# Kernel optimization log

Measured on AMD Instinct MI355X. Metric: run time of the kernel, lower is better.

## Reference

```python
import jax, jax.numpy as jnp
import numpy as np

B, C, E, K, HW = 8, 64, 4, 2, 128
LEAK = 0.2      # LeakyReLU slope in gate and experts
CLAMP = 0.8     # InvBlock clamp
EPS = 1e-5      # InstanceNorm eps


def _conv(x, w, b, pad):
    # x: [B,Ci,H,W], w: [Co,Ci,kh,kw] (OIHW)
    y = jax.lax.conv_general_dilated(x, w, (1, 1), [(pad, pad), (pad, pad)],
                                     dimension_numbers=('NCHW', 'OIHW', 'NCHW'))
    return y + b[None, :, None, None]


def _inorm(x, g, b):
    # InstanceNorm2d: per-sample, per-channel over H,W; biased variance
    m = x.mean(axis=(2, 3), keepdims=True)
    v = x.var(axis=(2, 3), keepdims=True)
    return (x - m) / jnp.sqrt(v + EPS) * g[None, :, None, None] + b[None, :, None, None]


def _hin(x, w1, b1, nw, nb, w2, b2):
    # HinResBlock with relu_slope=1 (d=1 passed by InvBlock) -> activations are identity
    r = _conv(x, w1, b1, 1)
    h1, h2 = jnp.split(r, 2, axis=1)
    r = jnp.concatenate([_inorm(h1, nw, nb), h2], axis=1)
    r = _conv(r, w2, b2, 1)
    return x + r


def setup_inputs() -> dict:
    key = jax.random.key(0)
    ks = jax.random.split(key, 20)
    s = 0.05
    Ch = C // 2
    inp = {
        'x': jax.random.normal(ks[0], (B, 2 * C, HW, HW), jnp.float32),
        # invertible 1x1 conv weight [2C, 2C]
        'winv': jax.random.normal(ks[1], (2 * C, 2 * C), jnp.float32) * s,
        # stacked HinResBlock params for F (idx 0), G (idx 1), H (idx 2)
        'blk_w1': jax.random.normal(ks[2], (3, C, C, 3, 3), jnp.float32) * s,
        'blk_b1': jax.random.normal(ks[3], (3, C), jnp.float32) * s,
        'blk_nw': jnp.ones((3, Ch), jnp.float32),
        'blk_nb': jnp.zeros((3, Ch), jnp.float32),
        'blk_w2': jax.random.normal(ks[4], (3, C, C, 3, 3), jnp.float32) * s,
        'blk_b2': jax.random.normal(ks[5], (3, C), jnp.float32) * s,
        # fuse 1x1 conv 2C -> C
        'fuse_w': jax.random.normal(ks[6], (C, 2 * C, 1, 1), jnp.float32) * s,
        'fuse_b': jax.random.normal(ks[7], (C,), jnp.float32) * s,
        # gate: fc0 (noise) random; fc1 weight zero-init per source, bias random
        'gw0': jax.random.normal(ks[8], (E, C), jnp.float32) * s,
        'gb0': jax.random.normal(ks[9], (E,), jnp.float32) * s,
        'gw1': jnp.zeros((E, C), jnp.float32),
        'gb1': jax.random.normal(ks[10], (E,), jnp.float32) * s,
        # stacked expert ConvProce params
        'ew1': jax.random.normal(ks[11], (E, C, C, 3, 3), jnp.float32) * s,
        'eb1': jax.random.normal(ks[12], (E, C), jnp.float32) * s,
        'ew2': jax.random.normal(ks[13], (E, C, C, 3, 3), jnp.float32) * s,
        'eb2': jax.random.normal(ks[14], (E, C), jnp.float32) * s,
    }
    return inp


def _forward(x, winv, blk_w1, blk_b1, blk_nw, blk_nb, blk_w2, blk_b2,
             fuse_w, fuse_b, gw0, gb0, gw1, gb1, ew1, eb1, ew2, eb2):
    # --- pre_fuse: InvBlock(2C, C) then 1x1 conv 2C->C ---
    z = jnp.einsum('oi,bihw->bohw', winv, x)  # invertible 1x1 conv (logdet unused)
    x1, x2 = z[:, :C], z[:, C:]
    hin = lambda i, h: _hin(h, blk_w1[i], blk_b1[i], blk_nw[i], blk_nb[i], blk_w2[i], blk_b2[i])
    y1 = x1 + hin(0, x2)                         # F
    s = CLAMP * (jax.nn.sigmoid(hin(2, y1)) * 2.0 - 1.0)  # H
    y2 = x2 * jnp.exp(s) + hin(1, y1)            # G
    xf = _conv(jnp.concatenate([y1, y2], axis=1), fuse_w, fuse_b, 0)  # [B,C,H,W]

    # --- gate ---
    g = jnp.max(xf, axis=(2, 3)) + jnp.mean(xf, axis=(2, 3))  # [B,C]
    lg = jax.nn.leaky_relu(g @ gw1.T + gb1, LEAK)             # [B,E]
    noise = jax.nn.softplus(g @ gw0.T + gb0)
    nm = noise.mean(axis=1, keepdims=True)
    ns = jnp.std(noise, axis=1, ddof=1, keepdims=True)        # torch.std is unbiased
    norm_noise = (noise - nm) / ns
    _, idx = jax.lax.top_k(lg + norm_noise, K)                # [B,K]
    mask = jnp.zeros((B, E), lg.dtype).at[jnp.arange(B)[:, None], idx].set(1.0)
    cof = jax.nn.softmax(jnp.where(mask > 0, lg, -jnp.inf), axis=1)  # [B,E]

    # --- experts: dense weighted combine (non-topk gates are exactly 0) ---
    def expert(w1, b1, w2, b2):
        h = jax.nn.leaky_relu(_conv(xf, w1, b1, 1), LEAK)
        return _conv(h, w2, b2, 1) + xf
    eouts = jax.vmap(expert)(ew1, eb1, ew2, eb2)  # [E,B,C,H,W]
    out = jnp.einsum('ebchw,be->bchw', eouts, cof)
    return out, cof


def reference(x, winv, blk_w1, blk_b1, blk_nw, blk_nb, blk_w2, blk_b2,
              fuse_w, fuse_b, gw0, gb0, gw1, gb1, ew1, eb1, ew2, eb2):
    return _forward(x, winv, blk_w1, blk_b1, blk_nw, blk_nb, blk_w2, blk_b2,
                    fuse_w, fuse_b, gw0, gb0, gw1, gb1, ew1, eb1, ew2, eb2)
```

## Files before the change

kernel.cpp:

```cpp
#include <hip/hip_runtime.h>
#include <cstddef>


#define HW2 16384
typedef short short8 __attribute__((ext_vector_type(8)));
typedef float f32x4 __attribute__((ext_vector_type(4)));
typedef unsigned short ushort_t;
typedef unsigned int uint_t;

enum { M_PLAIN = 0, M_ADD2 = 1, M_SIGEXP = 2, M_COUPLE = 3, M_LRELU = 4, M_EACC = 5 };

__device__ __forceinline__ float bf2f(ushort_t u) {
  return __uint_as_float(((uint_t)u) << 16);
}
__device__ __forceinline__ ushort_t f2bf(float f) {
  uint_t u = __float_as_uint(f);
  u += 0x7fffu + ((u >> 16) & 1u);
  return (ushort_t)(u >> 16);
}
__device__ __forceinline__ uint_t pack2(float a, float b) {
  return (uint_t)f2bf(a) | ((uint_t)f2bf(b) << 16);
}
__device__ __forceinline__ void ld4bf(const ushort_t* p, float* o) {
  uint2 d = *(const uint2*)p;
  o[0] = bf2f((ushort_t)(d.x & 0xffff)); o[1] = bf2f((ushort_t)(d.x >> 16));
  o[2] = bf2f((ushort_t)(d.y & 0xffff)); o[3] = bf2f((ushort_t)(d.y >> 16));
}
__device__ __forceinline__ void st4bf(ushort_t* p, const float* v) {
  uint2 st; st.x = pack2(v[0], v[1]); st.y = pack2(v[2], v[3]);
  *(uint2*)p = st;
}
__device__ __forceinline__ void gload_lds16(const void* g, void* l) {
  __builtin_amdgcn_global_load_lds(
      (const __attribute__((address_space(1))) void*)g,
      (__attribute__((address_space(3))) void*)l, 16, 0, 0);
}

__global__ void wtrans_kernel(const float* __restrict__ bw1, const float* __restrict__ bw2,
                              const float* __restrict__ ew1, const float* __restrict__ ew2,
                              ushort_t* __restrict__ wbuf) {
  int idx = blockIdx.x * 256 + threadIdx.x;
  int ci = idx & 63; int co = (idx >> 6) & 63;
  int rest = idx >> 12;
  int tap = rest % 9; int conv = rest / 9;
  const float* src;
  if (conv < 3)       src = bw1 + (size_t)conv * 36864;
  else if (conv < 6)  src = bw2 + (size_t)(conv - 3) * 36864;
  else if (conv < 10) src = ew1 + (size_t)(conv - 6) * 36864;
  else                src = ew2 + (size_t)(conv - 10) * 36864;
  float v = src[(co * 64 + ci) * 9 + tap];
  int n = co >> 4, col = co & 15;
  int h = ci >> 5, krow = (ci >> 3) & 3, e = ci & 7;
  int pos = conv * 36864 + (((tap * 2 + h) * 4 + n) << 9) + ((col << 2) + krow) * 8 + e;
  wbuf[pos] = f2bf(v);
}

__global__ void cvt_kernel(const float* __restrict__ s, ushort_t* __restrict__ d, int n) {
  int i = blockIdx.x * 256 + threadIdx.x;
  if (i < n) d[i] = f2bf(s[i]);
}

__global__ __launch_bounds__(256) void xtrans_kernel(const float* __restrict__ x,
                                                     ushort_t* __restrict__ xh) {
  int b = blockIdx.y;
  int oct = blockIdx.x >> 6;
  int p = ((blockIdx.x & 63) << 8) + threadIdx.x;
  short8 v;
#pragma unroll
  for (int j = 0; j < 8; ++j)
    v[j] = (short)f2bf(x[((size_t)(b * 128 + oct * 8 + j)) * HW2 + p]);
  *(short8*)(xh + ((size_t)b * HW2 + p) * 128 + oct * 8) = v;
}

template <int MODE, bool INORM>
__global__ __launch_bounds__(256, 3) void conv3_kernel(
    const ushort_t* __restrict__ in, int icstr, int icoff,
    const ushort_t* __restrict__ wgt, const float* __restrict__ bias,
    void* __restrict__ outv, int ocstr, int ocoff,
    const ushort_t* __restrict__ r1, int r1cstr, int r1off,
    const ushort_t* __restrict__ r2, int r2cstr, int r2off,
    const ushort_t* __restrict__ mul, int mcstr, int moff,
    const float* __restrict__ kh, const float* __restrict__ cof, int expert) {
  int b = blockIdx.y;
  float cv = 0.f; bool first = false;
  if (MODE == M_LRELU || MODE == M_EACC) {
    cv = cof[b * 4 + expert];
    if (cv == 0.f) return;
    if (MODE == M_EACC) {
      first = true;
      for (int e2 = 0; e2 < expert; ++e2) if (cof[b * 4 + e2] != 0.f) first = false;
    }
  }
  int tile = blockIdx.x;
  int ty0 = (tile >> 3) << 4;
  int tx0 = (tile & 7) << 4;
  int t = threadIdx.x;
  int lane = t & 63, w = t >> 6;

  __shared__ __align__(16) ushort_t sm[2592 * 8];
  char* smb = (char*)sm;

  if (!INORM) {
    for (int j = t; j < 2592; j += 256) {
      int row = j / 144, rem = j - row * 144;
      int xx = rem >> 3;
      int gy = ty0 + row - 1, gx = tx0 + xx - 1;
      if ((unsigned)gy >= 128u || (unsigned)gx >= 128u) {
        short8 z = {0, 0, 0, 0, 0, 0, 0, 0};
        *(short8*)(smb + (j << 4)) = z;
      }
    }
    for (int k = w; k < 41; k += 4) {
      int j = (k << 6) + lane;
      int row = j / 144, rem = j - row * 144;
      int xx = rem >> 3, octS = rem & 7;
      int oct = octS ^ (xx & 7);
      int gy = ty0 + row - 1, gx = tx0 + xx - 1;
      if (j < 2592 && (unsigned)gy < 128u && (unsigned)gx < 128u) {
        const ushort_t* gp =
            in + ((size_t)b * HW2 + (gy << 7) + gx) * icstr + icoff + oct * 8;
        gload_lds16(gp, smb + (k << 10));
      }
    }
  } else {
    short8 v[11];
#pragma unroll
    for (int k = 0; k < 11; ++k) {
      int j = t + (k << 8);
      short8 vv = {0, 0, 0, 0, 0, 0, 0, 0};
      if (j < 2592) {
        int row = j / 144, rem = j - row * 144;
        int xx = rem >> 3, octS = rem & 7;
        int oct = octS ^ (xx & 7);
        int gy = ty0 + row - 1, gx = tx0 + xx - 1;
        if ((unsigned)gy < 128u && (unsigned)gx < 128u) {
          vv = *(const short8*)(in + ((size_t)b * HW2 + (gy << 7) + gx) * icstr + icoff + oct * 8);
          if (oct < 4) {
            const float* khp = kh + (b * 32 + oct * 8) * 2;
#pragma unroll
            for (int jq = 0; jq < 8; ++jq) {
              float f = bf2f((ushort_t)vv[jq]);
              vv[jq] = (short)f2bf(f * khp[jq * 2] + khp[jq * 2 + 1]);
            }
          }
        }
      }
      v[k] = vv;
    }
#pragma unroll
    for (int k = 0; k < 11; ++k) {
      int j = t + (k << 8);
      if (j < 2592) *(short8*)(smb + (j << 4)) = v[k];
    }
  }
  __syncthreads();

  int col = lane & 15, krow = lane >> 4;
  int wofs = ((col << 2) + krow) * 8;
  f32x4 acc[4][4] = {};

#pragma unroll
  for (int tap = 0; tap < 9; ++tap) {
    const int dy = tap / 3, dx = tap - dy * 3;
#pragma unroll
    for (int h = 0; h < 2; ++h) {
      short8 af[4];
      const ushort_t* wbase = wgt + (((tap * 2 + h) * 4) << 9) + wofs;
#pragma unroll
      for (int n = 0; n < 4; ++n) af[n] = *(const short8*)(wbase + (n << 9));
      short8 bfr[4];
#pragma unroll
      for (int s = 0; s < 4; ++s) {
        int row = (w << 2) + s + dy, xx = col + dx;
        bfr[s] = *(const short8*)(smb +
                 (((row * 18 + xx) * 8 + ((h * 4 + krow) ^ (xx & 7))) << 4));
      }
#pragma unroll
      for (int s = 0; s < 4; ++s)
#pragma unroll
        for (int n = 0; n < 4; ++n)
          acc[s][n] = __builtin_amdgcn_mfma_f32_16x16x32_bf16(af[n], bfr[s], acc[s][n], 0, 0, 0);
    }
  }

#pragma unroll
  for (int s = 0; s < 4; ++s) {
    int py = ty0 + (w << 2) + s;
    size_t pix = (size_t)b * HW2 + (py << 7) + tx0 + col;
#pragma unroll
    for (int n = 0; n < 4; ++n) {
      int cb = n * 16 + krow * 4;
      float v[4];
#pragma unroll
      for (int r = 0; r < 4; ++r) v[r] = acc[s][n][r] + bias[cb + r];
      if (MODE == M_PLAIN) {
        st4bf((ushort_t*)outv + pix * ocstr + ocoff + cb, v);
      } else if (MODE == M_ADD2) {
        float a[4], bb[4];
        ld4bf(r1 + pix * r1cstr + r1off + cb, a);
        ld4bf(r2 + pix * r2cstr + r2off + cb, bb);
#pragma unroll
        for (int r = 0; r < 4; ++r) v[r] += a[r] + bb[r];
        st4bf((ushort_t*)outv + pix * ocstr + ocoff + cb, v);
      } else if (MODE == M_SIGEXP) {
        float a[4];
        ld4bf(r1 + pix * r1cstr + r1off + cb, a);
#pragma unroll
        for (int r = 0; r < 4; ++r) {
          float tt = v[r] + a[r];
          float sg = 1.f / (1.f + __expf(-tt));
          v[r] = __expf(1.6f * sg - 0.8f);
        }
        st4bf((ushort_t*)outv + pix * ocstr + ocoff + cb, v);
      } else if (MODE == M_COUPLE) {
        float a[4], bb[4], mm[4];
        ld4bf(r1 + pix * r1cstr + r1off + cb, a);
        ld4bf(r2 + pix * r2cstr + r2off + cb, bb);
        ld4bf(mul + pix * mcstr + moff + cb, mm);
#pragma unroll
        for (int r = 0; r < 4; ++r) v[r] += a[r] + bb[r] * mm[r];
        st4bf((ushort_t*)outv + pix * ocstr + ocoff + cb, v);
      } else if (MODE == M_LRELU) {
#pragma unroll
        for (int r = 0; r < 4; ++r) v[r] = v[r] > 0.f ? v[r] : 0.2f * v[r];
        st4bf((ushort_t*)outv + pix * ocstr + ocoff + cb, v);
      } else if (MODE == M_EACC) {
        float a[4];
        ld4bf(r1 + pix * r1cstr + r1off + cb, a);
        f32x4 val;
#pragma unroll
        for (int r = 0; r < 4; ++r) val[r] = cv * (v[r] + a[r]);
        float* ap = (float*)outv + pix * 64 + cb;
        if (first) *(f32x4*)ap = val;
        else { f32x4 old = *(f32x4*)ap; *(f32x4*)ap = old + val; }
      }
    }
  }
}

template <int NF>
__global__ __launch_bounds__(256, 3) void mm1_kernel(
    const ushort_t* __restrict__ in, int icstr,
    const ushort_t* __restrict__ wgt, const float* __restrict__ bias,
    ushort_t* __restrict__ out, int ocstr) {
  int b = blockIdx.y;
  int p0 = blockIdx.x << 7;
  int t = threadIdx.x, lane = t & 63, w = t >> 6;
  int col = lane & 15, krow = lane >> 4;
  size_t pixb = (size_t)b * HW2 + p0 + w * 32;
  short8 bfr[4][2];
#pragma unroll
  for (int kk = 0; kk < 4; ++kk)
#pragma unroll
    for (int s = 0; s < 2; ++s)
      bfr[kk][s] = *(const short8*)(in + (pixb + s * 16 + col) * icstr + kk * 32 + krow * 8);
  f32x4 acc[2][NF] = {};
#pragma unroll
  for (int kk = 0; kk < 4; ++kk) {
#pragma unroll
    for (int n = 0; n < NF; ++n) {
      short8 af = *(const short8*)(wgt + (n * 16 + col) * 128 + kk * 32 + krow * 8);
#pragma unroll
      for (int s = 0; s < 2; ++s)
        acc[s][n] = __builtin_amdgcn_mfma_f32_16x16x32_bf16(af, bfr[kk][s], acc[s][n], 0, 0, 0);
    }
  }
#pragma unroll
  for (int s = 0; s < 2; ++s) {
    size_t pix = pixb + s * 16 + col;
#pragma unroll
    for (int n = 0; n < NF; ++n) {
      int cb = n * 16 + krow * 4;
      float v[4];
#pragma unroll
      for (int r = 0; r < 4; ++r) v[r] = acc[s][n][r] + (bias ? bias[cb + r] : 0.f);
      st4bf(out + pix * ocstr + cb, v);
    }
  }
}

__global__ __launch_bounds__(256) void ireduce_kernel(const ushort_t* __restrict__ h,
                                                      float* __restrict__ part) {
  int b = blockIdx.y, chunk = blockIdx.x, t = threadIdx.x;
  int c = t & 31, g = t >> 5;
  float s = 0.f, q = 0.f;
  const ushort_t* base = h + ((size_t)b * HW2 + chunk * 512) * 64 + c;
  for (int i = 0; i < 64; ++i) {
    float f = bf2f(base[(g + i * 8) * 64]);
    s += f; q += f * f;
  }
  __shared__ float ls[8][32], lq[8][32];
  ls[g][c] = s; lq[g][c] = q;
  __syncthreads();
  if (t < 32) {
    float S = 0.f, Q = 0.f;
    for (int gg = 0; gg < 8; ++gg) { S += ls[gg][t]; Q += lq[gg][t]; }
    float* pp = part + ((b * 32 + chunk) * 32 + t) * 2;
    pp[0] = S; pp[1] = Q;
  }
}

__global__ void istat_kernel(const float* __restrict__ part, const float* __restrict__ nw,
                             const float* __restrict__ nb, float* __restrict__ kh) {
  int t = threadIdx.x; if (t >= 256) return;
  int b = t >> 5, c = t & 31;
  float S = 0.f, Q = 0.f;
  for (int ch = 0; ch < 32; ++ch) {
    const float* pp = part + ((b * 32 + ch) * 32 + c) * 2;
    S += pp[0]; Q += pp[1];
  }
  float m = S * (1.f / 16384.f);
  float var = Q * (1.f / 16384.f) - m * m;
  float k = nw[c] * rsqrtf(var + 1e-5f);
  kh[(b * 32 + c) * 2] = k;
  kh[(b * 32 + c) * 2 + 1] = nb[c] - m * k;
}

__global__ __launch_bounds__(256) void preduce_kernel(const ushort_t* __restrict__ xf,
                                                      float* __restrict__ part2) {
  int b = blockIdx.y, chunk = blockIdx.x, t = threadIdx.x;
  int c = t & 63, g = t >> 6;
  float s = 0.f, mx = -3.4e38f;
  const ushort_t* base = xf + ((size_t)b * HW2 + chunk * 512) * 64 + c;
  for (int i = 0; i < 128; ++i) {
    float f = bf2f(base[(g + i * 4) * 64]);
    s += f; mx = fmaxf(mx, f);
  }
  __shared__ float ls[4][64], lm[4][64];
  ls[g][c] = s; lm[g][c] = mx;
  __syncthreads();
  if (t < 64) {
    float S = ls[0][t] + ls[1][t] + ls[2][t] + ls[3][t];
    float M = fmaxf(fmaxf(lm[0][t], lm[1][t]), fmaxf(lm[2][t], lm[3][t]));
    float* pp = part2 + ((b * 32 + chunk) * 64 + t) * 2;
    pp[0] = S; pp[1] = M;
  }
}

__global__ void pool2_kernel(const float* __restrict__ part2, float* __restrict__ g) {
  int t = blockIdx.x * blockDim.x + threadIdx.x;
  if (t >= 512) return;
  int b = t >> 6, c = t & 63;
  float S = 0.f, M = -3.4e38f;
  for (int ch = 0; ch < 32; ++ch) {
    const float* pp = part2 + ((b * 32 + ch) * 64 + c) * 2;
    S += pp[0]; M = fmaxf(M, pp[1]);
  }
  g[t] = M + S * (1.f / 16384.f);
}

__global__ void gate_kernel(const float* __restrict__ g, const float* __restrict__ gw0,
                            const float* __restrict__ gb0, const float* __restrict__ gw1,
                            const float* __restrict__ gb1, float* __restrict__ cof) {
  int b = threadIdx.x;
  if (b >= 8) return;
  float lg[4], noise[4];
  for (int e = 0; e < 4; ++e) {
    float a0 = gb0[e], a1 = gb1[e];
    for (int c = 0; c < 64; ++c) {
      float gv = g[b * 64 + c];
      a0 += gv * gw0[e * 64 + c];
      a1 += gv * gw1[e * 64 + c];
    }
    lg[e] = a1 > 0.f ? a1 : 0.2f * a1;
    noise[e] = fmaxf(a0, 0.f) + log1pf(expf(-fabsf(a0)));
  }
  float nm = 0.25f * (noise[0] + noise[1] + noise[2] + noise[3]);
  float vs = 0.f;
  for (int e = 0; e < 4; ++e) { float d = noise[e] - nm; vs += d * d; }
  float ns = sqrtf(vs / 3.f);
  float sc[4];
  for (int e = 0; e < 4; ++e) sc[e] = lg[e] + (noise[e] - nm) / ns;
  int i1 = 0;
  for (int e = 1; e < 4; ++e) if (sc[e] > sc[i1]) i1 = e;
  int i2 = -1;
  for (int e = 0; e < 4; ++e) if (e != i1 && (i2 < 0 || sc[e] > sc[i2])) i2 = e;
  float mx = fmaxf(lg[i1], lg[i2]);
  float e1 = expf(lg[i1] - mx), e2 = expf(lg[i2] - mx);
  float d = e1 + e2;
  for (int e = 0; e < 4; ++e) cof[b * 4 + e] = 0.f;
  cof[b * 4 + i1] = e1 / d;
  cof[b * 4 + i2] = e2 / d;
}

__global__ __launch_bounds__(256) void nchw_kernel(const float* __restrict__ acc,
                                                   float* __restrict__ out) {
  int b = blockIdx.y, pix0 = blockIdx.x << 6, t = threadIdx.x;
  __shared__ float ts[64][68];
  for (int i = t; i < 1024; i += 256) {
    int px = i >> 4, grp = i & 15;
    f32x4 v = *(const f32x4*)(acc + ((size_t)b * HW2 + pix0 + px) * 64 + grp * 4);
    *(f32x4*)(&ts[px][grp * 4]) = v;
  }
  __syncthreads();
  int c = t >> 2, xg = t & 3;
#pragma unroll
  for (int j = 0; j < 4; ++j) {
    int px = xg * 16 + j * 4;
    f32x4 o;
#pragma unroll
    for (int k = 0; k < 4; ++k) o[k] = ts[px + k][c];
    *(f32x4*)(out + (((size_t)b * 64 + c) << 14) + pix0 + px) = o;
  }
}

extern "C" void kernel_launch(void* const* d_in, const int* in_sizes, int n_in,
                              void* d_out, int out_size, void* d_ws, size_t ws_size,
                              hipStream_t stream) {
  const float* x    = (const float*)d_in[0];
  const float* winv = (const float*)d_in[1];
  const float* w1   = (const float*)d_in[2];
  const float* b1   = (const float*)d_in[3];
  const float* nw   = (const float*)d_in[4];
  const float* nb   = (const float*)d_in[5];
  const float* w2   = (const float*)d_in[6];
  const float* b2   = (const float*)d_in[7];
  const float* fw   = (const float*)d_in[8];
  const float* fb   = (const float*)d_in[9];
  const float* gw0  = (const float*)d_in[10];
  const float* gb0  = (const float*)d_in[11];
  const float* gw1  = (const float*)d_in[12];
  const float* gb1  = (const float*)d_in[13];
  const float* ew1  = (const float*)d_in[14];
  const float* eb1  = (const float*)d_in[15];
  const float* ew2  = (const float*)d_in[16];
  const float* eb2  = (const float*)d_in[17];

  char* W = (char*)d_ws;
  ushort_t* A    = (ushort_t*)(W);
  ushort_t* Bz   = (ushort_t*)(W + 33554432);
  float*    accb = (float*)(W + 33554432);
  ushort_t* Ch   = (ushort_t*)(W + 67108864);
  ushort_t* Dx   = (ushort_t*)(W + 83886080);
  ushort_t* w3   = (ushort_t*)(W + 100663296);
  ushort_t* wmm  = (ushort_t*)(W + 101695488);
  ushort_t* wfu  = (ushort_t*)(W + 101728256);
  float* part1 = (float*)(W + 101744640);
  float* kh    = (float*)(W + 101810176);
  float* part2 = (float*)(W + 101812224);
  float* gbuf  = (float*)(W + 101943296);

  float* out = (float*)d_out;
  float* cof = out + (size_t)8 * 64 * HW2;

  const int WS3 = 36864;
  dim3 cg1(128, 8), cg3(64, 8), rg(32, 8);

  wtrans_kernel<<<2016, 256, 0, stream>>>(w1, w2, ew1, ew2, w3);
  cvt_kernel<<<64, 256, 0, stream>>>(winv, wmm, 16384);
  cvt_kernel<<<32, 256, 0, stream>>>(fw, wfu, 8192);
  xtrans_kernel<<<dim3(1024, 8), 256, 0, stream>>>(x, A);

  mm1_kernel<8><<<cg1, 256, 0, stream>>>(A, 128, wmm, nullptr, Bz, 128);

  conv3_kernel<M_PLAIN, false><<<cg3, 256, 0, stream>>>(Bz, 128, 64, w3 + 0 * WS3, b1,
      Ch, 64, 0, nullptr,0,0, nullptr,0,0, nullptr,0,0, kh, nullptr, 0);
  ireduce_kernel<<<rg, 256, 0, stream>>>(Ch, part1);
  istat_kernel<<<1, 256, 0, stream>>>(part1, nw, nb, kh);
  conv3_kernel<M_ADD2, true><<<cg3, 256, 0, stream>>>(Ch, 64, 0, w3 + 3 * WS3, b2,
      A, 128, 0, Bz, 128, 64, Bz, 128, 0, nullptr,0,0, kh, nullptr, 0);

  conv3_kernel<M_PLAIN, false><<<cg3, 256, 0, stream>>>(A, 128, 0, w3 + 2 * WS3, b1 + 128,
      Ch, 64, 0, nullptr,0,0, nullptr,0,0, nullptr,0,0, kh, nullptr, 0);
  ireduce_kernel<<<rg, 256, 0, stream>>>(Ch, part1);
  istat_kernel<<<1, 256, 0, stream>>>(part1, nw + 64, nb + 64, kh);
  conv3_kernel<M_SIGEXP, true><<<cg3, 256, 0, stream>>>(Ch, 64, 0, w3 + 5 * WS3, b2 + 128,
      Dx, 64, 0, A, 128, 0, nullptr,0,0, nullptr,0,0, kh, nullptr, 0);

  conv3_kernel<M_PLAIN, false><<<cg3, 256, 0, stream>>>(A, 128, 0, w3 + 1 * WS3, b1 + 64,
      Ch, 64, 0, nullptr,0,0, nullptr,0,0, nullptr,0,0, kh, nullptr, 0);
  ireduce_kernel<<<rg, 256, 0, stream>>>(Ch, part1);
  istat_kernel<<<1, 256, 0, stream>>>(part1, nw + 32, nb + 32, kh);
  conv3_kernel<M_COUPLE, true><<<cg3, 256, 0, stream>>>(Ch, 64, 0, w3 + 4 * WS3, b2 + 64,
      A, 128, 64, A, 128, 0, Bz, 128, 64, Dx, 64, 0, kh, nullptr, 0);

  mm1_kernel<4><<<cg1, 256, 0, stream>>>(A, 128, wfu, fb, Dx, 64);

  preduce_kernel<<<rg, 256, 0, stream>>>(Dx, part2);
  pool2_kernel<<<2, 256, 0, stream>>>(part2, gbuf);
  gate_kernel<<<1, 64, 0, stream>>>(gbuf, gw0, gb0, gw1, gb1, cof);

  for (int e = 0; e < 4; ++e) {
    conv3_kernel<M_LRELU, false><<<cg3, 256, 0, stream>>>(Dx, 64, 0, w3 + (6 + e) * WS3,
        eb1 + e * 64, Ch, 64, 0, nullptr,0,0, nullptr,0,0, nullptr,0,0, kh, cof, e);
    conv3_kernel<M_EACC, false><<<cg3, 256, 0, stream>>>(Ch, 64, 0, w3 + (10 + e) * WS3,
        eb2 + e * 64, (void*)accb, 64, 0, Dx, 64, 0, nullptr,0,0, nullptr,0,0, kh, cof, e);
  }

  nchw_kernel<<<dim3(256, 8), 256, 0, stream>>>(accb, out);
}
```

Measured before the change: 548.5 us.

## Give each wave a private halo tile in conv3 and drop block barrier

The 3x3 conv kernel now has each of its four waves stage its own 6x18-pixel halo region into a private slice of shared memory, instead of the whole block cooperatively loading one 18x18 tile. This removes the __syncthreads barrier, leaving only a per-wave vmcnt wait. In exchange the overlapping halo rows are loaded redundantly, shared memory per block grows from about 41KB to 55KB, and launch bounds drop from 3 to 2 blocks per CU for conv3 and mm1. The cost is lower occupancy and more global/LDS traffic.

```diff
diff --git a/kernel.cpp b/kernel.cpp
--- a/kernel.cpp
+++ b/kernel.cpp
@@ -73,7 +73,7 @@
 }
 
 template <int MODE, bool INORM>
-__global__ __launch_bounds__(256, 3) void conv3_kernel(
+__global__ __launch_bounds__(256, 2) void conv3_kernel(
     const ushort_t* __restrict__ in, int icstr, int icoff,
     const ushort_t* __restrict__ wgt, const float* __restrict__ bias,
     void* __restrict__ outv, int ocstr, int ocoff,
@@ -97,42 +97,51 @@
   int t = threadIdx.x;
   int lane = t & 63, w = t >> 6;
 
-  __shared__ __align__(16) ushort_t sm[2592 * 8];
-  char* smb = (char*)sm;
+  __shared__ __align__(16) ushort_t sm[4 * 864 * 8];
+  char* smb = (char*)sm + w * 13824;
+  int ry0 = ty0 + (w << 2) - 1;
 
   if (!INORM) {
-    for (int j = t; j < 2592; j += 256) {
-      int row = j / 144, rem = j - row * 144;
-      int xx = rem >> 3;
-      int gy = ty0 + row - 1, gx = tx0 + xx - 1;
-      if ((unsigned)gy >= 128u || (unsigned)gx >= 128u) {
-        short8 z = {0, 0, 0, 0, 0, 0, 0, 0};
-        *(short8*)(smb + (j << 4)) = z;
+#pragma unroll
+    for (int k = 0; k < 14; ++k) {
+      int j = (k << 6) + lane;
+      if (j < 864) {
+        int r = j / 144, rem = j - r * 144;
+        int xx = rem >> 3;
+        int gy = ry0 + r, gx = tx0 + xx - 1;
+        if ((unsigned)gy >= 128u || (unsigned)gx >= 128u) {
+          short8 z = {0, 0, 0, 0, 0, 0, 0, 0};
+          *(short8*)(smb + (j << 4)) = z;
+        }
       }
     }
-    for (int k = w; k < 41; k += 4) {
+#pragma unroll
+    for (int k = 0; k < 14; ++k) {
       int j = (k << 6) + lane;
-      int row = j / 144, rem = j - row * 144;
-      int xx = rem >> 3, octS = rem & 7;
-      int oct = octS ^ (xx & 7);
-      int gy = ty0 + row - 1, gx = tx0 + xx - 1;
-      if (j < 2592 && (unsigned)gy < 128u && (unsigned)gx < 128u) {
-        const ushort_t* gp =
-            in + ((size_t)b * HW2 + (gy << 7) + gx) * icstr + icoff + oct * 8;
-        gload_lds16(gp, smb + (k << 10));
-      }
-    }
-  } else {
-    short8 v[11];
-#pragma unroll
-    for (int k = 0; k < 11; ++k) {
-      int j = t + (k << 8);
-      short8 vv = {0, 0, 0, 0, 0, 0, 0, 0};
-      if (j < 2592) {
-        int row = j / 144, rem = j - row * 144;
+      if (j < 864) {
+        int r = j / 144, rem = j - r * 144;
         int xx = rem >> 3, octS = rem & 7;
         int oct = octS ^ (xx & 7);
-        int gy = ty0 + row - 1, gx = tx0 + xx - 1;
+        int gy = ry0 + r, gx = tx0 + xx - 1;
+        if ((unsigned)gy < 128u && (unsigned)gx < 128u) {
+          const ushort_t* gp =
+              in + ((size_t)b * HW2 + (gy << 7) + gx) * icstr + icoff + oct * 8;
+          gload_lds16(gp, smb + (k << 10));
+        }
+      }
+    }
+    asm volatile("s_waitcnt vmcnt(0)" ::: "memory");
+  } else {
+    short8 v[14];
+#pragma unroll
+    for (int k = 0; k < 14; ++k) {
+      int j = (k << 6) + lane;
+      short8 vv = {0, 0, 0, 0, 0, 0, 0, 0};
+      if (j < 864) {
+        int r = j / 144, rem = j - r * 144;
+        int xx = rem >> 3, octS = rem & 7;
+        int oct = octS ^ (xx & 7);
+        int gy = ry0 + r, gx = tx0 + xx - 1;
         if ((unsigned)gy < 128u && (unsigned)gx < 128u) {
           vv = *(const short8*)(in + ((size_t)b * HW2 + (gy << 7) + gx) * icstr + icoff + oct * 8);
           if (oct < 4) {
@@ -148,12 +157,11 @@
       v[k] = vv;
     }
 #pragma unroll
-    for (int k = 0; k < 11; ++k) {
-      int j = t + (k << 8);
-      if (j < 2592) *(short8*)(smb + (j << 4)) = v[k];
-    }
-  }
-  __syncthreads();
+    for (int k = 0; k < 14; ++k) {
+      int j = (k << 6) + lane;
+      if (j < 864) *(short8*)(smb + (j << 4)) = v[k];
+    }
+  }
 
   int col = lane & 15, krow = lane >> 4;
   int wofs = ((col << 2) + krow) * 8;
@@ -171,9 +179,9 @@
       short8 bfr[4];
 #pragma unroll
       for (int s = 0; s < 4; ++s) {
-        int row = (w << 2) + s + dy, xx = col + dx;
+        int r = s + dy, xx = col + dx;
         bfr[s] = *(const short8*)(smb +
-                 (((row * 18 + xx) * 8 + ((h * 4 + krow) ^ (xx & 7))) << 4));
+                 (((r * 18 + xx) * 8 + ((h * 4 + krow) ^ (xx & 7))) << 4));
       }
 #pragma unroll
       for (int s = 0; s < 4; ++s)
@@ -239,7 +247,7 @@
 }
 
 template <int NF>
-__global__ __launch_bounds__(256, 3) void mm1_kernel(
+__global__ __launch_bounds__(256, 2) void mm1_kernel(
     const ushort_t* __restrict__ in, int icstr,
     const ushort_t* __restrict__ wgt, const float* __restrict__ bias,
     ushort_t* __restrict__ out, int ocstr) {
```

Measured after the change: 599.8 us. 9.4% more time.

## Batch top-k expert convs and fuse weighted second conv with NCHW output

Applied to the files above, without the earlier changes.

The gate kernel now emits the two selected expert indices per sample. The first expert conv runs as a single launch over a z-dimension of two selected experts instead of four per-expert launches with early exit. A new efin kernel computes both selected experts' second conv into one accumulator: it pre-scales the hidden activations by the gate coefficient while loading to LDS, then adds the combined bias and residual and writes NCHW fp32 output directly. This removes the fp32 accumulation buffer read-modify-write and the separate transpose kernel. Rounding the coefficient-scaled activations to bf16 changes numerics slightly, and launch bounds drop from 3 to 2 blocks per CU.

```diff
diff --git a/kernel.cpp b/kernel.cpp
--- a/kernel.cpp
+++ b/kernel.cpp
@@ -8,7 +8,7 @@
 typedef unsigned short ushort_t;
 typedef unsigned int uint_t;
 
-enum { M_PLAIN = 0, M_ADD2 = 1, M_SIGEXP = 2, M_COUPLE = 3, M_LRELU = 4, M_EACC = 5 };
+enum { M_PLAIN = 0, M_ADD2 = 1, M_SIGEXP = 2, M_COUPLE = 3, M_LRELU = 4 };
 
 __device__ __forceinline__ float bf2f(ushort_t u) {
   return __uint_as_float(((uint_t)u) << 16);
@@ -73,23 +73,20 @@
 }
 
 template <int MODE, bool INORM>
-__global__ __launch_bounds__(256, 3) void conv3_kernel(
+__global__ __launch_bounds__(256, 2) void conv3_kernel(
     const ushort_t* __restrict__ in, int icstr, int icoff,
     const ushort_t* __restrict__ wgt, const float* __restrict__ bias,
     void* __restrict__ outv, int ocstr, int ocoff,
     const ushort_t* __restrict__ r1, int r1cstr, int r1off,
     const ushort_t* __restrict__ r2, int r2cstr, int r2off,
     const ushort_t* __restrict__ mul, int mcstr, int moff,
-    const float* __restrict__ kh, const float* __restrict__ cof, int expert) {
+    const float* __restrict__ kh, const int* __restrict__ eidx) {
   int b = blockIdx.y;
-  float cv = 0.f; bool first = false;
-  if (MODE == M_LRELU || MODE == M_EACC) {
-    cv = cof[b * 4 + expert];
-    if (cv == 0.f) return;
-    if (MODE == M_EACC) {
-      first = true;
-      for (int e2 = 0; e2 < expert; ++e2) if (cof[b * 4 + e2] != 0.f) first = false;
-    }
+  if (MODE == M_LRELU) {
+    int e = eidx[b * 2 + (int)blockIdx.z];
+    wgt += (size_t)(6 + e) * 36864;
+    bias += e * 64;
+    outv = (void*)((ushort_t*)outv + (size_t)blockIdx.z * 8388608);
   }
   int tile = blockIdx.x;
   int ty0 = (tile >> 3) << 4;
@@ -224,22 +221,108 @@
 #pragma unroll
         for (int r = 0; r < 4; ++r) v[r] = v[r] > 0.f ? v[r] : 0.2f * v[r];
         st4bf((ushort_t*)outv + pix * ocstr + ocoff + cb, v);
-      } else if (MODE == M_EACC) {
-        float a[4];
-        ld4bf(r1 + pix * r1cstr + r1off + cb, a);
-        f32x4 val;
-#pragma unroll
-        for (int r = 0; r < 4; ++r) val[r] = cv * (v[r] + a[r]);
-        float* ap = (float*)outv + pix * 64 + cb;
-        if (first) *(f32x4*)ap = val;
-        else { f32x4 old = *(f32x4*)ap; *(f32x4*)ap = old + val; }
+      }
+    }
+  }
+}
+
+__global__ __launch_bounds__(256) void efin_kernel(
+    const ushort_t* __restrict__ hbase,
+    const ushort_t* __restrict__ xf,
+    const ushort_t* __restrict__ wgt14,
+    const float* __restrict__ eb2,
+    const int* __restrict__ eidx, const float* __restrict__ cof,
+    float* __restrict__ out) {
+  int b = blockIdx.y;
+  int tile = blockIdx.x;
+  int ty0 = (tile >> 3) << 3;
+  int tx0 = (tile & 7) << 4;
+  int t = threadIdx.x, lane = t & 63, w = t >> 6;
+  int col = lane & 15, krow = lane >> 4;
+  __shared__ __align__(16) ushort_t sm[1440 * 8];
+  char* smb = (char*)sm;
+  int e0 = eidx[b * 2], e1 = eidx[b * 2 + 1];
+  float c0 = cof[b * 4 + e0], c1 = cof[b * 4 + e1];
+  int wofs = ((col << 2) + krow) * 8;
+  f32x4 acc[2][4] = {};
+
+  for (int s = 0; s < 2; ++s) {
+    float cs = s ? c1 : c0;
+    const ushort_t* hsrc = hbase + (size_t)s * 8388608;
+    const ushort_t* wgt = wgt14 + (size_t)(10 + (s ? e1 : e0)) * 36864;
+    if (s) __syncthreads();
+    short8 v[6];
+#pragma unroll
+    for (int k = 0; k < 6; ++k) {
+      int j = t + (k << 8);
+      short8 vv = {0, 0, 0, 0, 0, 0, 0, 0};
+      if (j < 1440) {
+        int row = j / 144, rem = j - row * 144;
+        int xx = rem >> 3, octS = rem & 7;
+        int oct = octS ^ (xx & 7);
+        int gy = ty0 + row - 1, gx = tx0 + xx - 1;
+        if ((unsigned)gy < 128u && (unsigned)gx < 128u) {
+          vv = *(const short8*)(hsrc + ((size_t)b * HW2 + (gy << 7) + gx) * 64 + oct * 8);
+#pragma unroll
+          for (int jq = 0; jq < 8; ++jq)
+            vv[jq] = (short)f2bf(bf2f((ushort_t)vv[jq]) * cs);
+        }
+      }
+      v[k] = vv;
+    }
+#pragma unroll
+    for (int k = 0; k < 6; ++k) {
+      int j = t + (k << 8);
+      if (j < 1440) *(short8*)(smb + (j << 4)) = v[k];
+    }
+    __syncthreads();
+#pragma unroll
+    for (int tap = 0; tap < 9; ++tap) {
+      const int dy = tap / 3, dx = tap - dy * 3;
+#pragma unroll
+      for (int h = 0; h < 2; ++h) {
+        short8 af[4];
+        const ushort_t* wbase = wgt + (((tap * 2 + h) * 4) << 9) + wofs;
+#pragma unroll
+        for (int n = 0; n < 4; ++n) af[n] = *(const short8*)(wbase + (n << 9));
+        short8 bfr[2];
+#pragma unroll
+        for (int ss = 0; ss < 2; ++ss) {
+          int row = (w << 1) + ss + dy, xx = col + dx;
+          bfr[ss] = *(const short8*)(smb +
+                   (((row * 18 + xx) * 8 + ((h * 4 + krow) ^ (xx & 7))) << 4));
+        }
+#pragma unroll
+        for (int ss = 0; ss < 2; ++ss)
+#pragma unroll
+          for (int n = 0; n < 4; ++n)
+            acc[ss][n] = __builtin_amdgcn_mfma_f32_16x16x32_bf16(af[n], bfr[ss], acc[ss][n], 0, 0, 0);
+      }
+    }
+  }
+
+#pragma unroll
+  for (int ss = 0; ss < 2; ++ss) {
+    int py = ty0 + (w << 1) + ss;
+    size_t pnh = (size_t)b * HW2 + (py << 7) + tx0 + col;
+#pragma unroll
+    for (int n = 0; n < 4; ++n) {
+      int cb = n * 16 + krow * 4;
+      float xv[4];
+      ld4bf(xf + pnh * 64 + cb, xv);
+#pragma unroll
+      for (int r = 0; r < 4; ++r) {
+        int c = cb + r;
+        float bb = c0 * eb2[e0 * 64 + c] + c1 * eb2[e1 * 64 + c];
+        out[(((size_t)b * 64 + c) << 14) + (py << 7) + tx0 + col] =
+            acc[ss][n][r] + bb + xv[r];
       }
     }
   }
 }
 
 template <int NF>
-__global__ __launch_bounds__(256, 3) void mm1_kernel(
+__global__ __launch_bounds__(256, 2) void mm1_kernel(
     const ushort_t* __restrict__ in, int icstr,
     const ushort_t* __restrict__ wgt, const float* __restrict__ bias,
     ushort_t* __restrict__ out, int ocstr) {
@@ -351,7 +434,8 @@
 
 __global__ void gate_kernel(const float* __restrict__ g, const float* __restrict__ gw0,
                             const float* __restrict__ gb0, const float* __restrict__ gw1,
-                            const float* __restrict__ gb1, float* __restrict__ cof) {
+                            const float* __restrict__ gb1, float* __restrict__ cof,
+                            int* __restrict__ eidx) {
   int b = threadIdx.x;
   if (b >= 8) return;
   float lg[4], noise[4];
@@ -381,27 +465,8 @@
   for (int e = 0; e < 4; ++e) cof[b * 4 + e] = 0.f;
   cof[b * 4 + i1] = e1 / d;
   cof[b * 4 + i2] = e2 / d;
-}
-
-__global__ __launch_bounds__(256) void nchw_kernel(const float* __restrict__ acc,
-                                                   float* __restrict__ out) {
-  int b = blockIdx.y, pix0 = blockIdx.x << 6, t = threadIdx.x;
-  __shared__ float ts[64][68];
-  for (int i = t; i < 1024; i += 256) {
-    int px = i >> 4, grp = i & 15;
-    f32x4 v = *(const f32x4*)(acc + ((size_t)b * HW2 + pix0 + px) * 64 + grp * 4);
-    *(f32x4*)(&ts[px][grp * 4]) = v;
-  }
-  __syncthreads();
-  int c = t >> 2, xg = t & 3;
-#pragma unroll
-  for (int j = 0; j < 4; ++j) {
-    int px = xg * 16 + j * 4;
-    f32x4 o;
-#pragma unroll
-    for (int k = 0; k < 4; ++k) o[k] = ts[px + k][c];
-    *(f32x4*)(out + (((size_t)b * 64 + c) << 14) + pix0 + px) = o;
-  }
+  eidx[b * 2] = i1;
+  eidx[b * 2 + 1] = i2;
 }
 
 extern "C" void kernel_launch(void* const* d_in, const int* in_sizes, int n_in,
@@ -429,7 +494,6 @@
   char* W = (char*)d_ws;
   ushort_t* A    = (ushort_t*)(W);
   ushort_t* Bz   = (ushort_t*)(W + 33554432);
-  float*    accb = (float*)(W + 33554432);
   ushort_t* Ch   = (ushort_t*)(W + 67108864);
   ushort_t* Dx   = (ushort_t*)(W + 83886080);
   ushort_t* w3   = (ushort_t*)(W + 100663296);
@@ -439,6 +503,7 @@
   float* kh    = (float*)(W + 101810176);
   float* part2 = (float*)(W + 101812224);
   float* gbuf  = (float*)(W + 101943296);
+  int*   eidx  = (int*)(W + 101945344);
 
   float* out = (float*)d_out;
   float* cof = out + (size_t)8 * 64 * HW2;
@@ -454,38 +519,33 @@
   mm1_kernel<8><<<cg1, 256, 0, stream>>>(A, 128, wmm, nullptr, Bz, 128);
 
   conv3_kernel<M_PLAIN, false><<<cg3, 256, 0, stream>>>(Bz, 128, 64, w3 + 0 * WS3, b1,
-      Ch, 64, 0, nullptr,0,0, nullptr,0,0, nullptr,0,0, kh, nullptr, 0);
+      Ch, 64, 0, nullptr,0,0, nullptr,0,0, nullptr,0,0, kh, nullptr);
   ireduce_kernel<<<rg, 256, 0, stream>>>(Ch, part1);
   istat_kernel<<<1, 256, 0, stream>>>(part1, nw, nb, kh);
   conv3_kernel<M_ADD2, true><<<cg3, 256, 0, stream>>>(Ch, 64, 0, w3 + 3 * WS3, b2,
-      A, 128, 0, Bz, 128, 64, Bz, 128, 0, nullptr,0,0, kh, nullptr, 0);
+      A, 128, 0, Bz, 128, 64, Bz, 128, 0, nullptr,0,0, kh, nullptr);
 
   conv3_kernel<M_PLAIN, false><<<cg3, 256, 0, stream>>>(A, 128, 0, w3 + 2 * WS3, b1 + 128,
-      Ch, 64, 0, nullptr,0,0, nullptr,0,0, nullptr,0,0, kh, nullptr, 0);
+      Ch, 64, 0, nullptr,0,0, nullptr,0,0, nullptr,0,0, kh, nullptr);
   ireduce_kernel<<<rg, 256, 0, stream>>>(Ch, part1);
   istat_kernel<<<1, 256, 0, stream>>>(part1, nw + 64, nb + 64, kh);
   conv3_kernel<M_SIGEXP, true><<<cg3, 256, 0, stream>>>(Ch, 64, 0, w3 + 5 * WS3, b2 + 128,
-      Dx, 64, 0, A, 128, 0, nullptr,0,0, nullptr,0,0, kh, nullptr, 0);
+      Dx, 64, 0, A, 128, 0, nullptr,0,0, nullptr,0,0, kh, nullptr);
 
   conv3_kernel<M_PLAIN, false><<<cg3, 256, 0, stream>>>(A, 128, 0, w3 + 1 * WS3, b1 + 64,
-      Ch, 64, 0, nullptr,0,0, nullptr,0,0, nullptr,0,0, kh, nullptr, 0);
+      Ch, 64, 0, nullptr,0,0, nullptr,0,0, nullptr,0,0, kh, nullptr);
   ireduce_kernel<<<rg, 256, 0, stream>>>(Ch, part1);
   istat_kernel<<<1, 256, 0, stream>>>(part1, nw + 32, nb + 32, kh);
   conv3_kernel<M_COUPLE, true><<<cg3, 256, 0, stream>>>(Ch, 64, 0, w3 + 4 * WS3, b2 + 64,
-      A, 128, 64, A, 128, 0, Bz, 128, 64, Dx, 64, 0, kh, nullptr, 0);
+      A, 128, 64, A, 128, 0, Bz, 128, 64, Dx, 64, 0, kh, nullptr);
 
   mm1_kernel<4><<<cg1, 256, 0, stream>>>(A, 128, wfu, fb, Dx, 64);
 
   preduce_kernel<<<rg, 256, 0, stream>>>(Dx, part2);
   pool2_kernel<<<2, 256, 0, stream>>>(part2, gbuf);
-  gate_kernel<<<1, 64, 0, stream>>>(gbuf, gw0, gb0, gw1, gb1, cof);
-
-  for (int e = 0; e < 4; ++e) {
-    conv3_kernel<M_LRELU, false><<<cg3, 256, 0, stream>>>(Dx, 64, 0, w3 + (6 + e) * WS3,
-        eb1 + e * 64, Ch, 64, 0, nullptr,0,0, nullptr,0,0, nullptr,0,0, kh, cof, e);
-    conv3_kernel<M_EACC, false><<<cg3, 256, 0, stream>>>(Ch, 64, 0, w3 + (10 + e) * WS3,
-        eb2 + e * 64, (void*)accb, 64, 0, Dx, 64, 0, nullptr,0,0, nullptr,0,0, kh, cof, e);
-  }
-
-  nchw_kernel<<<dim3(256, 8), 256, 0, stream>>>(accb, out);
-}
+  gate_kernel<<<1, 64, 0, stream>>>(gbuf, gw0, gb0, gw1, gb1, cof, eidx);
+
+  conv3_kernel<M_LRELU, false><<<dim3(64, 8, 2), 256, 0, stream>>>(Dx, 64, 0, w3, eb1,
+      A, 64, 0, nullptr,0,0, nullptr,0,0, nullptr,0,0, kh, eidx);
+  efin_kernel<<<cg1, 256, 0, stream>>>(A, Dx, w3, eb2, eidx, cof, out);
+}
```

After: 476.4 us. -13.1%, faster.
